# Kernel optimization log

Measured on AMD Instinct MI355X. Metric: run time of the kernel, lower is better.

The kernel has to match this reference:

```python
import jax, jax.numpy as jnp
import numpy as np
import math

B, N, D_MODEL, H, D_HEAD = 2, 2048, 1024, 16, 64
EPS = 1e-6

def setup_inputs() -> dict:
    key = jax.random.key(0)
    ks = jax.random.split(key, 6)
    s = 1.0 / math.sqrt(D_MODEL)
    return {
        "X": jax.random.normal(ks[0], (B, N, D_MODEL), dtype=jnp.float32),
        "Wq": jax.random.normal(ks[1], (D_MODEL, H * D_HEAD), dtype=jnp.float32) * s,
        "Wk": jax.random.normal(ks[2], (D_MODEL, H * D_HEAD), dtype=jnp.float32) * s,
        "Wv": jax.random.normal(ks[3], (D_MODEL, H * D_HEAD), dtype=jnp.float32) * s,
        "Wo": jax.random.normal(ks[4], (H * D_HEAD, D_MODEL), dtype=jnp.float32) * s,
        "bo": jnp.zeros((D_MODEL,), dtype=jnp.float32),
    }

def reference(X, Wq, Wk, Wv, Wo, bo):
    b, n, _ = X.shape
    # project and split heads -> [b, h, n, d_head]
    def heads(Y):
        return Y.reshape(b, n, H, D_HEAD).transpose(0, 2, 1, 3)
    Q = heads(X @ Wq)
    K = heads(X @ Wk)
    V = heads(X @ Wv)
    # per-head L2 normalization of Q and K
    Q = Q / (jnp.linalg.norm(Q, axis=-1, keepdims=True) + EPS)
    K = K / (jnp.linalg.norm(K, axis=-1, keepdims=True) + EPS)
    # scores [b, h, n, n]
    A = jnp.einsum("bhqd,bhkd->bhqk", Q, K) / math.sqrt(D_HEAD)
    causal = jnp.triu(jnp.ones((n, n), dtype=bool), k=1)
    A = jnp.where(causal, -jnp.inf, A)
    A = jax.nn.softmax(A, axis=-1)
    V_hat = jnp.einsum("bhqk,bhkd->bhqd", A, V)
    V_hat = V_hat.transpose(0, 2, 1, 3).reshape(b, n, H * D_HEAD)
    return V_hat @ Wo + bo
```

## Files before the change

### kernel.cpp

```cpp
#include <hip/hip_runtime.h>
#include <hip/hip_bf16.h>
#include <math.h>

#define BATCH 2
#define NSEQ  2048
#define DM    1024
#define NH    16
#define DH    64
#define EPS_N 1e-6f

typedef unsigned short u16;
typedef __attribute__((ext_vector_type(8))) short short8;
typedef __attribute__((ext_vector_type(8))) unsigned short u16x8;
typedef __attribute__((ext_vector_type(4))) unsigned short u16x4;
typedef __attribute__((ext_vector_type(4))) float f32x4;

__device__ __forceinline__ u16 f2bf(float x) {
  __hip_bfloat16 h = __float2bfloat16(x);
  return *reinterpret_cast<u16*>(&h);
}

__device__ __forceinline__ void gl_lds16(const u16* g, u16* lds_base) {
  __builtin_amdgcn_global_load_lds(
      (__attribute__((address_space(1))) void*)g,
      (__attribute__((address_space(3))) void*)lds_base, 16, 0, 0);
}

__global__ __launch_bounds__(256) void prep(
    const float* __restrict__ X,
    const float* __restrict__ w0, const float* __restrict__ w1,
    const float* __restrict__ w2, const float* __restrict__ w3,
    u16* __restrict__ Xb, u16* __restrict__ WT) {
  const int id = blockIdx.x, tid = threadIdx.x;
  if (id >= 1024) {
    size_t base = ((size_t)(id - 1024) * 256 + tid) * 8;
    float4 f0 = *(const float4*)&X[base];
    float4 f1 = *(const float4*)&X[base + 4];
    u16x8 v;
    v[0] = f2bf(f0.x); v[1] = f2bf(f0.y); v[2] = f2bf(f0.z); v[3] = f2bf(f0.w);
    v[4] = f2bf(f1.x); v[5] = f2bf(f1.y); v[6] = f2bf(f1.z); v[7] = f2bf(f1.w);
    *(u16x8*)&Xb[base] = v;
    return;
  }
  const int z = id >> 8, xy = id & 255, bx = xy & 15, by = xy >> 4;
  const float* in = (z == 0) ? w0 : (z == 1) ? w1 : (z == 2) ? w2 : w3;
  u16* o = WT + (size_t)z * DM * DM;
  __shared__ u16 T[64][65];
  const int n0 = bx * 64, k0 = by * 64;
  #pragma unroll
  for (int i = 0; i < 4; i++) {
    int c = tid + 256 * i, row = c >> 4, col4 = c & 15;
    float4 f = *(const float4*)&in[(size_t)(k0 + row) * DM + n0 + col4 * 4];
    T[row][col4 * 4 + 0] = f2bf(f.x);
    T[row][col4 * 4 + 1] = f2bf(f.y);
    T[row][col4 * 4 + 2] = f2bf(f.z);
    T[row][col4 * 4 + 3] = f2bf(f.w);
  }
  __syncthreads();
  #pragma unroll
  for (int i = 0; i < 2; i++) {
    int c = tid + 256 * i, row = c >> 3, col8 = c & 7;
    u16x8 v;
    #pragma unroll
    for (int e = 0; e < 8; e++) v[e] = T[col8 * 8 + e][row];
    *(u16x8*)&o[(size_t)(n0 + row) * DM + k0 + col8 * 8] = v;
  }
}

#define GEMM64x128_MAINLOOP(Aptr, Btptr)                                       \
  __shared__ u16 As[64 * 64];                                                  \
  __shared__ u16 Bs[128 * 64];                                                 \
  const int tid = threadIdx.x, w = tid >> 6, lane = tid & 63;                  \
  const int ml = lane & 15, quad = lane >> 4;                                  \
  const int m0 = blockIdx.y * 64, n0 = blockIdx.x * 128;                       \
  const int wm = w & 1, wn = w >> 1;                                           \
  const int srow = lane >> 3;                      \
  const int scol = ((lane & 7) ^ srow) * 8;         \
  f32x4 acc[2][4];                                                             \
  _Pragma("unroll") for (int mi = 0; mi < 2; mi++)                             \
    _Pragma("unroll") for (int ni = 0; ni < 4; ni++)                           \
      _Pragma("unroll") for (int e = 0; e < 4; e++) acc[mi][ni][e] = 0.f;      \
  for (int k0 = 0; k0 < DM; k0 += 64) {                                        \
    __syncthreads();                                                           \
    _Pragma("unroll") for (int L = 0; L < 2; L++) {                            \
      int I = w * 2 + L;                                    \
      gl_lds16(Aptr + (size_t)(m0 + I * 8 + srow) * DM + k0 + scol,            \
               As + I * 512);                                                  \
    }                                                                          \
    _Pragma("unroll") for (int L = 0; L < 4; L++) {                            \
      int I = w * 4 + L;                                   \
      gl_lds16(Btptr + (size_t)(n0 + I * 8 + srow) * DM + k0 + scol,           \
               Bs + I * 512);                                                  \
    }                                                                          \
    __syncthreads();                                                           \
    _Pragma("unroll") for (int kk = 0; kk < 64; kk += 32) {                    \
      const int kc = kk >> 3;                          \
      short8 am[2], bn[4];                                                     \
      _Pragma("unroll") for (int i = 0; i < 2; i++) {                          \
        int ra = wm * 32 + i * 16 + ml;                                        \
        am[i] = *(const short8*)&As[ra * 64 + (((quad + kc) ^ (ra & 7)) * 8)]; \
      }                                                                        \
      _Pragma("unroll") for (int i = 0; i < 4; i++) {                          \
        int rb = wn * 64 + i * 16 + ml;                                        \
        bn[i] = *(const short8*)&Bs[rb * 64 + (((quad + kc) ^ (rb & 7)) * 8)]; \
      }                                                                        \
      _Pragma("unroll") for (int mi = 0; mi < 2; mi++)                         \
        _Pragma("unroll") for (int ni = 0; ni < 4; ni++)                       \
          acc[mi][ni] = __builtin_amdgcn_mfma_f32_16x16x32_bf16(               \
              am[mi], bn[ni], acc[mi][ni], 0, 0, 0);                           \
    }                                                                          \
  }

__global__ __launch_bounds__(256) void gemm_qkv128(
    const u16* __restrict__ Xb, const u16* __restrict__ WT,
    u16* __restrict__ Qo, u16* __restrict__ Ko, u16* __restrict__ Vt) {
  const u16* Bt = WT + (size_t)blockIdx.z * DM * DM;
  GEMM64x128_MAINLOOP(Xb, Bt)
  const int z = blockIdx.z;
  if (z < 2) {
    u16* OutQK = (z == 0) ? Qo : Ko;
    const float qsc = (z == 0) ? 0.125f : 1.0f;
    const int h = (n0 >> 6) + wn;
    #pragma unroll
    for (int mi = 0; mi < 2; mi++) {
      int mrow0 = m0 + wm * 32 + mi * 16 + quad * 4;
      int b = mrow0 >> 11, tok0 = mrow0 & (NSEQ - 1);
      #pragma unroll
      for (int r = 0; r < 4; r++) {
        float ss = 0.f;
        #pragma unroll
        for (int ni = 0; ni < 4; ni++) ss += acc[mi][ni][r] * acc[mi][ni][r];
        ss += __shfl_xor(ss, 1, 64);
        ss += __shfl_xor(ss, 2, 64);
        ss += __shfl_xor(ss, 4, 64);
        ss += __shfl_xor(ss, 8, 64);
        float sc = qsc / (sqrtf(ss) + EPS_N);
        #pragma unroll
        for (int ni = 0; ni < 4; ni++)
          OutQK[((size_t)(b * NH + h) * NSEQ + tok0 + r) * DH + ni * 16 + ml] =
              f2bf(acc[mi][ni][r] * sc);
      }
    }
  } else {
    #pragma unroll
    for (int mi = 0; mi < 2; mi++) {
      int mrow0 = m0 + wm * 32 + mi * 16 + quad * 4;
      int b = mrow0 >> 11, tok0 = mrow0 & (NSEQ - 1);
      #pragma unroll
      for (int ni = 0; ni < 4; ni++) {
        int n = n0 + wn * 64 + ni * 16 + ml;
        int h = n >> 6, d = n & 63;
        u16x4 pk;
        #pragma unroll
        for (int r = 0; r < 4; r++) pk[r] = f2bf(acc[mi][ni][r]);
        *(u16x4*)&Vt[((size_t)(b * NH + h) * DH + d) * NSEQ + tok0] = pk;
      }
    }
  }
}

__global__ __launch_bounds__(256) void gemm_proj128(
    const u16* __restrict__ A, const u16* __restrict__ BtW,
    const float* __restrict__ bias, float* __restrict__ out) {
  GEMM64x128_MAINLOOP(A, BtW)
  #pragma unroll
  for (int ni = 0; ni < 4; ni++) {
    int n = n0 + wn * 64 + ni * 16 + ml;
    float bz = bias[n];
    #pragma unroll
    for (int mi = 0; mi < 2; mi++) {
      int mrow0 = m0 + wm * 32 + mi * 16 + quad * 4;
      #pragma unroll
      for (int r = 0; r < 4; r++)
        out[(size_t)(mrow0 + r) * DM + n] = acc[mi][ni][r] + bz;
    }
  }
}

__global__ __launch_bounds__(256) void flash_attn(
    const u16* __restrict__ Qb, const u16* __restrict__ Kb,
    const u16* __restrict__ Vt, u16* __restrict__ vhat) {
  const int tid = threadIdx.x, w = tid >> 6, lane = tid & 63;
  const int ml = lane & 15, quad = lane >> 4;
  const int wq = w & 1, wk = w >> 1;
  const int bh = blockIdx.x;
  const int bb = bh >> 4, hb = bh & 15;
  const int pair = blockIdx.y;
  const u16* Qh = Qb + (size_t)bh * NSEQ * DH;
  const u16* Kh = Kb + (size_t)bh * NSEQ * DH;
  const u16* Vth = Vt + (size_t)bh * DH * NSEQ;

  __shared__ u16 Ks [64 * 64];
  __shared__ u16 VsT[64 * 64];
  __shared__ u16 Ps [4][16][40];
  __shared__ float Os[2][16][66];
  __shared__ float Ls[2][16];

  const int srow8 = lane >> 3;
  const int sch   = lane & 7;
  const int sslot = sch ^ srow8;

  for (int ph = 0; ph < 2; ph++) {
    const int qb32 = ph ? (63 - pair) : pair;
    const int q0 = qb32 * 32;
    const int ntiles = (qb32 >> 1) + 1;

    short8 aq[2];
    #pragma unroll
    for (int c = 0; c < 2; c++)
      aq[c] = *(const short8*)&Qh[(size_t)(q0 + wq * 16 + ml) * DH + c * 32 + quad * 8];

    f32x4 oacc[4];
    #pragma unroll
    for (int n = 0; n < 4; n++)
      #pragma unroll
      for (int e = 0; e < 4; e++) oacc[n][e] = 0.f;
    float l_[4] = {0.f, 0.f, 0.f, 0.f};

    u16x8 kreg[2], vreg[2];
    #pragma unroll
    for (int i = 0; i < 2; i++) {
      int slab = w * 2 + i;
      kreg[i] = *(const u16x8*)&Kh[(size_t)(slab * 8 + srow8) * DH + sch * 8];
      vreg[i] = *(const u16x8*)&Vth[(size_t)(slab * 8 + srow8) * NSEQ + sch * 8];
    }

    for (int t = 0; t < ntiles; t++) {
      const int j0 = t * 64;
      __syncthreads();
      #pragma unroll
      for (int i = 0; i < 2; i++) {
        int slab = w * 2 + i;
        *(u16x8*)&Ks [(slab * 8 + srow8) * 64 + sslot * 8] = kreg[i];
        *(u16x8*)&VsT[(slab * 8 + srow8) * 64 + sslot * 8] = vreg[i];
      }
      __syncthreads();

      if (t + 1 < ntiles) {
        const int j1 = j0 + 64;
        #pragma unroll
        for (int i = 0; i < 2; i++) {
          int slab = w * 2 + i;
          kreg[i] = *(const u16x8*)&Kh[(size_t)(j1 + slab * 8 + srow8) * DH + sch * 8];
          vreg[i] = *(const u16x8*)&Vth[(size_t)(slab * 8 + srow8) * NSEQ + j1 + sch * 8];
        }
      }

      f32x4 sacc[2];
      #pragma unroll
      for (int n = 0; n < 2; n++)
        #pragma unroll
        for (int e = 0; e < 4; e++) sacc[n][e] = 0.f;
      #pragma unroll
      for (int c = 0; c < 2; c++)
        #pragma unroll
        for (int n = 0; n < 2; n++) {
          int kr = wk * 32 + n * 16 + ml;
          short8 bf = *(const short8*)&Ks[kr * 64 + (((c * 4 + quad) ^ (kr & 7)) * 8)];
          sacc[n] = __builtin_amdgcn_mfma_f32_16x16x32_bf16(aq[c], bf, sacc[n], 0, 0, 0);
        }

      const bool lastt = (t == ntiles - 1);
      float p[2][4];
      #pragma unroll
      for (int n = 0; n < 2; n++) {
        int j = j0 + wk * 32 + n * 16 + ml;
        #pragma unroll
        for (int r = 0; r < 4; r++) {
          int q = q0 + wq * 16 + quad * 4 + r;
          float e = __expf(sacc[n][r]);
          p[n][r] = (lastt && j > q) ? 0.f : e;
          l_[r] += p[n][r];
        }
      }

      #pragma unroll
      for (int n = 0; n < 2; n++)
        #pragma unroll
        for (int r = 0; r < 4; r++)
          Ps[w][quad * 4 + r][n * 16 + ml] = f2bf(p[n][r]);

      short8 ap = *(const short8*)&Ps[w][ml][quad * 8];
      #pragma unroll
      for (int n = 0; n < 4; n++) {
        int dr = n * 16 + ml;
        short8 bv = *(const short8*)&VsT[dr * 64 + (((wk * 4 + quad) ^ (dr & 7)) * 8)];
        oacc[n] = __builtin_amdgcn_mfma_f32_16x16x32_bf16(ap, bv, oacc[n], 0, 0, 0);
      }
    }

    float lred[4];
    #pragma unroll
    for (int r = 0; r < 4; r++) {
      float lv = l_[r];
      lv += __shfl_xor(lv, 1, 64);
      lv += __shfl_xor(lv, 2, 64);
      lv += __shfl_xor(lv, 4, 64);
      lv += __shfl_xor(lv, 8, 64);
      lred[r] = lv;
    }
    if (wk == 0) {
      #pragma unroll
      for (int n = 0; n < 4; n++)
        #pragma unroll
        for (int r = 0; r < 4; r++)
          Os[wq][quad * 4 + r][n * 16 + ml] = oacc[n][r];
      if (ml == 0) {
        #pragma unroll
        for (int r = 0; r < 4; r++) Ls[wq][quad * 4 + r] = lred[r];
      }
    }
    __syncthreads();
    if (wk == 1) {
      #pragma unroll
      for (int r = 0; r < 4; r++) {
        float inv = 1.f / (lred[r] + Ls[wq][quad * 4 + r]);
        int q = q0 + wq * 16 + quad * 4 + r;
        #pragma unroll
        for (int n = 0; n < 4; n++) {
          float o = oacc[n][r] + Os[wq][quad * 4 + r][n * 16 + ml];
          vhat[((size_t)(bb * NSEQ + q)) * DM + hb * DH + n * 16 + ml] =
              f2bf(o * inv);
        }
      }
    }
    __syncthreads();
  }
}

extern "C" void kernel_launch(void* const* d_in, const int* in_sizes, int n_in,
                              void* d_out, int out_size, void* d_ws, size_t ws_size,
                              hipStream_t stream) {
  const float* X  = (const float*)d_in[0];
  const float* Wq = (const float*)d_in[1];
  const float* Wk = (const float*)d_in[2];
  const float* Wv = (const float*)d_in[3];
  const float* Wo = (const float*)d_in[4];
  const float* bo = (const float*)d_in[5];
  float* out = (float*)d_out;

  const size_t NE = (size_t)BATCH * NSEQ * DM;
  u16* Qb   = (u16*)d_ws;
  u16* Kb   = Qb + NE;
  u16* Vt   = Kb + NE;
  u16* XbVh = Vt + NE;
  u16* WT   = XbVh + NE;

  prep        <<<dim3(3072),      256, 0, stream>>>(X, Wq, Wk, Wv, Wo, XbVh, WT);
  gemm_qkv128 <<<dim3(8, 64, 3),  256, 0, stream>>>(XbVh, WT, Qb, Kb, Vt);
  flash_attn  <<<dim3(32, 32),    256, 0, stream>>>(Qb, Kb, Vt, XbVh);
  gemm_proj128<<<dim3(8, 64, 1),  256, 0, stream>>>(XbVh, WT + 3 * (size_t)DM * DM,
                                                    bo, out);
}
```

Measured before the change: 187.5 us.

## Grow flash attention query tile to 64 rows with 8 waves per block

The attention kernel moves from 4 waves handling 32 query rows to 8 waves handling 64 query rows per block. Each K/V tile staged in shared memory is now reused by twice as many queries, and the grid is halved. Each wave loads one slab instead of two. The hidden part of the kernel (masking, softmax, P/O reduction through Ps/Os/Ls) must handle the new wave indexing. If it does not, the change may be incomplete. Fewer blocks and the coarser diagonal tiles could also hurt load balance and occupancy.

```diff
diff --git a/kernel.cpp b/kernel.cpp
--- a/kernel.cpp
+++ b/kernel.cpp
@@ -177,33 +177,33 @@
   }
 }
 
-__global__ __launch_bounds__(256) void flash_attn(
+__global__ __launch_bounds__(512) void flash_attn(
     const u16* __restrict__ Qb, const u16* __restrict__ Kb,
     const u16* __restrict__ Vt, u16* __restrict__ vhat) {
   const int tid = threadIdx.x, w = tid >> 6, lane = tid & 63;
   const int ml = lane & 15, quad = lane >> 4;
-  const int wq = w & 1, wk = w >> 1;
+  const int wq = w & 3, wk = w >> 2;
   const int bh = blockIdx.x;
   const int bb = bh >> 4, hb = bh & 15;
-  const int pair = blockIdx.y;
+  const int pairY = blockIdx.y;
   const u16* Qh = Qb + (size_t)bh * NSEQ * DH;
   const u16* Kh = Kb + (size_t)bh * NSEQ * DH;
   const u16* Vth = Vt + (size_t)bh * DH * NSEQ;
 
   __shared__ u16 Ks [64 * 64];
   __shared__ u16 VsT[64 * 64];
-  __shared__ u16 Ps [4][16][40];
-  __shared__ float Os[2][16][66];
-  __shared__ float Ls[2][16];
+  __shared__ u16 Ps [8][16][40];
+  __shared__ float Os[4][16][66];
+  __shared__ float Ls[4][16];
 
   const int srow8 = lane >> 3;
   const int sch   = lane & 7;
   const int sslot = sch ^ srow8;
 
   for (int ph = 0; ph < 2; ph++) {
-    const int qb32 = ph ? (63 - pair) : pair;
-    const int q0 = qb32 * 32;
-    const int ntiles = (qb32 >> 1) + 1;
+    const int qb64 = ph ? (31 - pairY) : pairY;
+    const int q0 = qb64 * 64;
+    const int ntiles = qb64 + 1;
 
     short8 aq[2];
     #pragma unroll
@@ -217,33 +217,21 @@
       for (int e = 0; e < 4; e++) oacc[n][e] = 0.f;
     float l_[4] = {0.f, 0.f, 0.f, 0.f};
 
-    u16x8 kreg[2], vreg[2];
-    #pragma unroll
-    for (int i = 0; i < 2; i++) {
-      int slab = w * 2 + i;
-      kreg[i] = *(const u16x8*)&Kh[(size_t)(slab * 8 + srow8) * DH + sch * 8];
-      vreg[i] = *(const u16x8*)&Vth[(size_t)(slab * 8 + srow8) * NSEQ + sch * 8];
-    }
+    u16x8 kreg, vreg;
+    kreg = *(const u16x8*)&Kh[(size_t)(w * 8 + srow8) * DH + sch * 8];
+    vreg = *(const u16x8*)&Vth[(size_t)(w * 8 + srow8) * NSEQ + sch * 8];
 
     for (int t = 0; t < ntiles; t++) {
       const int j0 = t * 64;
       __syncthreads();
-      #pragma unroll
-      for (int i = 0; i < 2; i++) {
-        int slab = w * 2 + i;
-        *(u16x8*)&Ks [(slab * 8 + srow8) * 64 + sslot * 8] = kreg[i];
-        *(u16x8*)&VsT[(slab * 8 + srow8) * 64 + sslot * 8] = vreg[i];
-      }
+      *(u16x8*)&Ks [(w * 8 + srow8) * 64 + sslot * 8] = kreg;
+      *(u16x8*)&VsT[(w * 8 + srow8) * 64 + sslot * 8] = vreg;
       __syncthreads();
 
       if (t + 1 < ntiles) {
         const int j1 = j0 + 64;
-        #pragma unroll
-        for (int i = 0; i < 2; i++) {
-          int slab = w * 2 + i;
-          kreg[i] = *(const u16x8*)&Kh[(size_t)(j1 + slab * 8 + srow8) * DH + sch * 8];
-          vreg[i] = *(const u16x8*)&Vth[(size_t)(slab * 8 + srow8) * NSEQ + j1 + sch * 8];
-        }
+        kreg = *(const u16x8*)&Kh[(size_t)(j1 + w * 8 + srow8) * DH + sch * 8];
+        vreg = *(const u16x8*)&Vth[(size_t)(w * 8 + srow8) * NSEQ + j1 + sch * 8];
       }
 
       f32x4 sacc[2];
@@ -348,7 +336,7 @@
 
   prep        <<<dim3(3072),      256, 0, stream>>>(X, Wq, Wk, Wv, Wo, XbVh, WT);
   gemm_qkv128 <<<dim3(8, 64, 3),  256, 0, stream>>>(XbVh, WT, Qb, Kb, Vt);
-  flash_attn  <<<dim3(32, 32),    256, 0, stream>>>(Qb, Kb, Vt, XbVh);
+  flash_attn  <<<dim3(32, 16),    512, 0, stream>>>(Qb, Kb, Vt, XbVh);
   gemm_proj128<<<dim3(8, 64, 1),  256, 0, stream>>>(XbVh, WT + 3 * (size_t)DM * DM,
                                                     bo, out);
 }
```

After: 182.2 us. 1.03x faster.
